# Optimization experiments

Hardware: AMD Instinct MI355X
Metric: run time of the kernel (lower is better)

## Reference

```python
import jax, jax.numpy as jnp
import numpy as np

B0, C0, H0, W0 = 32, 512, 64, 64  # x shape; L = C0 = d_model
DC = 32   # c_increase (per-direction inner dim)
NS = 16   # d_state
RK = 32   # dt_rank = ceil(512/16)


def setup_inputs() -> dict:
    key = jax.random.key(0)
    ks = jax.random.split(key, 8)
    x = jax.random.normal(ks[0], (B0, C0, H0, W0), jnp.float32)
    xc_proj_weight = jax.random.normal(ks[1], (2, RK + 2 * NS, DC), jnp.float32) * 0.05
    dtc_projs_weight = jax.random.uniform(ks[2], (2, DC, RK), jnp.float32, -RK ** -0.5, RK ** -0.5)
    # inv-softplus of dt sampled log-uniform in [1e-3, 1e-1]
    dt = jnp.exp(jax.random.uniform(ks[3], (2, DC)) * (np.log(0.1) - np.log(0.001)) + np.log(0.001))
    dtc_projs_bias = dt + jnp.log(-jnp.expm1(-dt))
    Ac_logs = jnp.log(jnp.tile(jnp.arange(1, NS + 1, dtype=jnp.float32), (2 * DC, 1)))  # [2D, N]
    Dcs = jnp.ones((2 * DC,), jnp.float32)
    w_cin = jax.random.normal(ks[4], (DC, 2), jnp.float32) * 0.5    # Conv2d(2, DC, 1) weight
    bn_gamma = jnp.ones((DC,), jnp.float32)
    bn_beta = jnp.zeros((DC,), jnp.float32)
    bn_mean = jnp.zeros((DC,), jnp.float32)
    bn_var = jnp.ones((DC,), jnp.float32)
    w_cout = jax.random.normal(ks[5], (DC,), jnp.float32) * 0.2     # Conv2d(DC, 1, 1) weight
    ln_gamma = jnp.ones((C0,), jnp.float32)
    ln_beta = jnp.zeros((C0,), jnp.float32)
    return dict(x=x, xc_proj_weight=xc_proj_weight, dtc_projs_weight=dtc_projs_weight,
                dtc_projs_bias=dtc_projs_bias, Ac_logs=Ac_logs, Dcs=Dcs, w_cin=w_cin,
                bn_gamma=bn_gamma, bn_beta=bn_beta, bn_mean=bn_mean, bn_var=bn_var,
                w_cout=w_cout, ln_gamma=ln_gamma, ln_beta=ln_beta)


def _selective_scan(u, delta, A, Bs, Cs, D, delta_bias):
    # u, delta: [B, 2D, L]; A: [2D, N]; Bs, Cs: [B, 2, N, L] (K=2 groups); D, delta_bias: [2D]
    B, KD, L = u.shape
    d_per = KD // Bs.shape[1]
    delta = jax.nn.softplus(delta + delta_bias[None, :, None])
    Bg = jnp.repeat(Bs, d_per, axis=1)  # [B, 2D, N, L] (group = d // d_per)
    Cg = jnp.repeat(Cs, d_per, axis=1)
    dA = jnp.exp(delta[:, :, None, :] * A[None, :, :, None])      # [B, 2D, N, L]
    dBu = delta[:, :, None, :] * Bg * u[:, :, None, :]            # [B, 2D, N, L]

    def step(h, inp):
        dA_l, dBu_l = inp
        h = dA_l * h + dBu_l
        return h, h

    h0 = jnp.zeros((B, KD, dA.shape[2]), u.dtype)
    _, hs = jax.lax.scan(step, h0, (jnp.moveaxis(dA, 3, 0), jnp.moveaxis(dBu, 3, 0)))  # [L, B, 2D, N]
    y = jnp.einsum('lbdn,bdnl->bdl', hs, Cg) + D[None, :, None] * u
    return y


def reference(x, xc_proj_weight, dtc_projs_weight, dtc_projs_bias, Ac_logs, Dcs,
              w_cin, bn_gamma, bn_beta, bn_mean, bn_var, w_cout, ln_gamma, ln_beta):
    B, C, H, W = x.shape
    L = C
    avg = jnp.mean(x, axis=(2, 3))          # [B, C]
    mx = jnp.max(x, axis=(2, 3))            # [B, C]
    xsc = jnp.stack([avg, mx], axis=1)       # [B, 2, C]
    # 1x1 conv (2 -> DC) over 'spatial' dim C, + BatchNorm(eval) + GELU
    h = jnp.einsum('bic,di->bdc', xsc, w_cin)  # [B, DC, L]
    h = (h - bn_mean[None, :, None]) * jax.lax.rsqrt(bn_var + 1e-5)[None, :, None]
    h = h * bn_gamma[None, :, None] + bn_beta[None, :, None]
    h = jax.nn.gelu(h, approximate=False)
    # bidirectional stacking
    xk = jnp.stack([h, jnp.flip(h, axis=-1)], axis=1)  # [B, 2, DC, L]
    dbl = jnp.einsum('bkdl,kcd->bkcl', xk, xc_proj_weight)  # [B, 2, R+2N, L]
    dts, Bs, Cs = dbl[:, :, :RK], dbl[:, :, RK:RK + NS], dbl[:, :, RK + NS:]
    dts = jnp.einsum('bkrl,kdr->bkdl', dts, dtc_projs_weight)  # [B, 2, DC, L]
    u = xk.reshape(B, 2 * DC, L)
    delta = dts.reshape(B, 2 * DC, L)
    A = -jnp.exp(Ac_logs)  # [2D, N]
    out_y = _selective_scan(u, delta, A, Bs, Cs, Dcs, dtc_projs_bias.reshape(-1))
    out_y = out_y.reshape(B, 2, DC, L)
    y = out_y[:, 0] + jnp.flip(out_y[:, 1], axis=-1)  # [B, DC, L]
    # 1x1 conv (DC -> 1, no bias) + GELU
    y = jax.nn.gelu(jnp.einsum('bdl,d->bl', y, w_cout), approximate=False)  # [B, L]
    # LayerNorm over channel dim (d_model = C)
    mu = jnp.mean(y, axis=-1, keepdims=True)
    var = jnp.var(y, axis=-1, keepdims=True)
    attn = (y - mu) * jax.lax.rsqrt(var + 1e-5) * ln_gamma[None, :] + ln_beta[None, :]
    attn = attn[:, :, None, None]  # [B, C, 1, 1]
    return x + x * attn
```

## Files before the change

kernel.cpp:

```cpp
#include <hip/hip_runtime.h>
#include <math.h>

#define B0 32
#define C0 512
#define HW 4096
#define DC 32
#define NS 16
#define RK 32
#define L  512
#define KD 64
#define CB 64
#define NCH (L / CB)
#define FSTR 16

#define LOAD_ACQ(p)    __hip_atomic_load((p), __ATOMIC_ACQUIRE, __HIP_MEMORY_SCOPE_AGENT)
#define LOAD_RLX(p)    __hip_atomic_load((p), __ATOMIC_RELAXED, __HIP_MEMORY_SCOPE_AGENT)
#define STORE_RLX(p,v) __hip_atomic_store((p), (v), __ATOMIC_RELAXED, __HIP_MEMORY_SCOPE_AGENT)
#define STORE_REL(p,v) __hip_atomic_store((p), (v), __ATOMIC_RELEASE, __HIP_MEMORY_SCOPE_AGENT)

__device__ __forceinline__ float gelu_exact(float x) {
    return 0.5f * x * (1.0f + erff(x * 0.70710678118654752f));
}
__device__ __forceinline__ float softplus_f(float x) {
    float ax = fabsf(x);
    return fmaxf(x, 0.0f) + log1pf(expf(-ax));
}

__global__ __launch_bounds__(256) void pool_kernel(const float* __restrict__ x,
                                                   float* __restrict__ avg,
                                                   float* __restrict__ mx) {
    int row = blockIdx.x;
    const float4* xr = (const float4*)(x + (size_t)row * HW);
    int tid = threadIdx.x;
    float s = 0.f, m = -INFINITY;
#pragma unroll
    for (int i = 0; i < 4; ++i) {
        float4 v = xr[tid + i * 256];
        s += v.x + v.y + v.z + v.w;
        m = fmaxf(m, fmaxf(fmaxf(v.x, v.y), fmaxf(v.z, v.w)));
    }
    for (int off = 32; off > 0; off >>= 1) {
        s += __shfl_down(s, off, 64);
        m = fmaxf(m, __shfl_down(m, off, 64));
    }
    __shared__ float ss[4], sm[4];
    int wave = tid >> 6;
    if ((tid & 63) == 0) { ss[wave] = s; sm[wave] = m; }
    __syncthreads();
    if (tid == 0) {
        s = ss[0] + ss[1] + ss[2] + ss[3];
        m = fmaxf(fmaxf(sm[0], sm[1]), fmaxf(sm[2], sm[3]));
        avg[row] = s * (1.0f / HW);
        mx[row] = m;
    }
}

__global__ __launch_bounds__(512) void mid_kernel(
    const float* __restrict__ avg, const float* __restrict__ mx,
    const float* __restrict__ w_cin,
    const float* __restrict__ bn_g, const float* __restrict__ bn_b,
    const float* __restrict__ bn_m, const float* __restrict__ bn_v,
    const float* __restrict__ xcw, const float* __restrict__ dtw,
    const float* __restrict__ dtb,
    const float* __restrict__ Ac_logs, const float* __restrict__ Dcs,
    const float* __restrict__ w_cout,
    float* __restrict__ carry,
    int* __restrict__ flags,
    float* __restrict__ ybl2)
{
    __shared__ float sW[64 * DC];
    __shared__ float sPW[DC * RK];
    __shared__ float sh_c[DC * (CB + 1)];
    __shared__ float sde[DC * (CB + 1)];
    __shared__ float sdtred[DC * (CB + 1)];
    __shared__ float sB[CB * (NS + 1)];
    __shared__ float sC[CB * (NS + 1)];

    float* sdt = sdtred;
    float* red = sdtred;

    int bk = blockIdx.x & 63;
    int c  = blockIdx.x >> 6;
    int k = bk & 1;
    int b = bk >> 1;
    int lidx = bk * NCH + c;
    int tid = threadIdx.x;

    for (int i = tid; i < 64 * DC; i += 512) sW[i]  = xcw[k * 64 * DC + i];
    for (int i = tid; i < DC * RK; i += 512) sPW[i] = dtw[k * DC * RK + i];

    int l0 = k ? (L - (c + 1) * CB) : c * CB;

    for (int i = tid; i < DC * CB; i += 512) {
        int d = i >> 6, ll = i & (CB - 1);
        int gl = l0 + ll;
        float a = avg[b * C0 + gl], m = mx[b * C0 + gl];
        float v = a * w_cin[d * 2] + m * w_cin[d * 2 + 1];
        v = (v - bn_m[d]) * rsqrtf(bn_v[d] + 1e-5f);
        v = v * bn_g[d] + bn_b[d];
        sh_c[d * (CB + 1) + ll] = gelu_exact(v);
    }
    __syncthreads();

    for (int idx = tid; idx < 64 * CB; idx += 512) {
        int cc = idx >> 6, ll = idx & (CB - 1);
        float acc = 0.f;
#pragma unroll
        for (int d = 0; d < DC; ++d) acc += sh_c[d * (CB + 1) + ll] * sW[cc * DC + d];
        if (cc < RK) sdt[cc * CB + ll] = acc;
        else if (cc < RK + NS) sB[ll * (NS + 1) + (cc - RK)] = acc;
        else sC[ll * (NS + 1) + (cc - RK - NS)] = acc;
    }
    __syncthreads();

    for (int idx = tid; idx < DC * CB; idx += 512) {
        int d = idx >> 6, ll = idx & (CB - 1);
        float acc = dtb[k * DC + d];
#pragma unroll
        for (int r = 0; r < RK; ++r) acc += sdt[r * CB + ll] * sPW[d * RK + r];
        sde[d * (CB + 1) + ll] = softplus_f(acc);
    }
    __syncthreads();

    int d_s = tid >> 4;
    int n_s = tid & 15;
    int kd  = k * DC + d_s;
    float A = -expf(Ac_logs[kd * NS + n_s]);
    float hloc = 0.f, sdsum = 0.f;
#pragma unroll 4
    for (int sl = 0; sl < CB; ++sl) {
        int ll = k ? (CB - 1 - sl) : sl;
        float de = sde[d_s * (CB + 1) + ll];
        float u  = sh_c[d_s * (CB + 1) + ll];
        float Bv = sB[ll * (NS + 1) + n_s];
        hloc = expf(de * A) * hloc + de * Bv * u;
        sdsum += de;
    }

    float cin = 0.f;
    if (c > 0) {
        const int* fprev = flags + (lidx - 1) * FSTR;
        if (tid == 0) {
            while (LOAD_ACQ(fprev) == 0) __builtin_amdgcn_s_sleep(2);
        }
        __syncthreads();
        cin = LOAD_RLX(carry + (size_t)(lidx - 1) * (DC * NS) + tid);
    }
    if (c < NCH - 1) {
        float cout = expf(A * sdsum) * cin + hloc;
        STORE_RLX(carry + (size_t)lidx * (DC * NS) + tid, cout);
        __syncthreads();
        if (tid == 0) STORE_REL(flags + lidx * FSTR, 1);
    }

    float w  = w_cout[d_s];
    float Dv = Dcs[kd];
    float hs = cin;
#pragma unroll 4
    for (int sl = 0; sl < CB; ++sl) {
        int ll = k ? (CB - 1 - sl) : sl;
        float de = sde[d_s * (CB + 1) + ll];
        float u  = sh_c[d_s * (CB + 1) + ll];
        float Bv = sB[ll * (NS + 1) + n_s];
        float Cv = sC[ll * (NS + 1) + n_s];
        hs = expf(de * A) * hs + de * Bv * u;
        float contrib = hs * Cv;
        contrib += __shfl_xor(contrib, 1, 16);
        contrib += __shfl_xor(contrib, 2, 16);
        contrib += __shfl_xor(contrib, 4, 16);
        contrib += __shfl_xor(contrib, 8, 16);
        if (n_s == 0) red[d_s * (CB + 1) + ll] = w * (contrib + Dv * u);
    }
    __syncthreads();

    if (tid < CB) {
        int ll = tid;
        float acc = 0.f;
#pragma unroll
        for (int dd = 0; dd < DC; ++dd) acc += red[dd * (CB + 1) + ll];
        ybl2[(size_t)bk * L + l0 + ll] = acc;
    }
}

__global__ __launch_bounds__(512) void epi_kernel(const float* __restrict__ ybl2,
                                                  const float* __restrict__ ln_g,
                                                  const float* __restrict__ ln_b,
                                                  float* __restrict__ attn) {
    int b = blockIdx.x;
    int l = threadIdx.x;
    float y = gelu_exact(ybl2[(size_t)(b * 2) * L + l] + ybl2[(size_t)(b * 2 + 1) * L + l]);
    float s = y, s2 = y * y;
    for (int off = 32; off > 0; off >>= 1) {
        s += __shfl_down(s, off, 64);
        s2 += __shfl_down(s2, off, 64);
    }
    __shared__ float ss[8], ss2[8];
    __shared__ float smu, srv;
    int wave = l >> 6;
    if ((l & 63) == 0) { ss[wave] = s; ss2[wave] = s2; }
    __syncthreads();
    if (l == 0) {
        float ts = 0.f, ts2 = 0.f;
#pragma unroll
        for (int i = 0; i < 8; ++i) { ts += ss[i]; ts2 += ss2[i]; }
        float mu = ts * (1.0f / L);
        float var = ts2 * (1.0f / L) - mu * mu;
        smu = mu;
        srv = rsqrtf(var + 1e-5f);
    }
    __syncthreads();
    attn[b * C0 + l] = (y - smu) * srv * ln_g[l] + ln_b[l];
}

__global__ __launch_bounds__(256) void gate_kernel(const float* __restrict__ x,
                                                   const float* __restrict__ attn,
                                                   float* __restrict__ out) {
    const float4* x4 = (const float4*)x;
    float4* o4 = (float4*)out;
    size_t base = (size_t)blockIdx.x * 2048 + threadIdx.x;
#pragma unroll
    for (int i = 0; i < 8; ++i) {
        size_t t = base + (size_t)i * 256;
        float4 v = x4[t];
        float a = 1.0f + attn[t >> 10];
        v.x *= a; v.y *= a; v.z *= a; v.w *= a;
        o4[t] = v;
    }
}

extern "C" void kernel_launch(void* const* d_in, const int* in_sizes, int n_in,
                              void* d_out, int out_size, void* d_ws, size_t ws_size,
                              hipStream_t stream) {
    const float* x     = (const float*)d_in[0];
    const float* xcw   = (const float*)d_in[1];
    const float* dtw   = (const float*)d_in[2];
    const float* dtb   = (const float*)d_in[3];
    const float* Aclog = (const float*)d_in[4];
    const float* Dcs   = (const float*)d_in[5];
    const float* wcin  = (const float*)d_in[6];
    const float* bng   = (const float*)d_in[7];
    const float* bnb   = (const float*)d_in[8];
    const float* bnm   = (const float*)d_in[9];
    const float* bnv   = (const float*)d_in[10];
    const float* wcout = (const float*)d_in[11];
    const float* lng   = (const float*)d_in[12];
    const float* lnb   = (const float*)d_in[13];
    float* out = (float*)d_out;

    float* ws = (float*)d_ws;
    float* avg   = ws;
    float* mx    = ws + 16384;
    float* ybl2  = ws + 32768;
    float* attn  = ws + 65536;
    float* carry = ws + 81920;
    int*   flags = (int*)(ws + 344064);

    pool_kernel<<<B0 * C0, 256, 0, stream>>>(x, avg, mx);
    hipMemsetAsync(flags, 0, (size_t)64 * NCH * FSTR * sizeof(int), stream);
    mid_kernel<<<64 * NCH, 512, 0, stream>>>(avg, mx, wcin, bng, bnb, bnm, bnv,
                                             xcw, dtw, dtb, Aclog, Dcs, wcout,
                                             carry, flags, ybl2);
    epi_kernel<<<B0, 512, 0, stream>>>(ybl2, lng, lnb, attn);
    gate_kernel<<<(B0 * C0 * HW / 4) / 2048, 256, 0, stream>>>(x, attn, out);
}
```

Measured before the change: 583.2 us.

## Replace serial chunk carry chain with independent publish and prefix recombination

Each chunk block now publishes its local end state and summed delta right away, without waiting for its predecessor. Consumers wait on all earlier chunk flags and rebuild the carry-in by combining those partial states in sequence. This removes the serial chunk-to-chunk dependency chain in the scan. The flag reset moves from a separate memset into the pool kernel, which drops one launch. In exchange, later chunks do more global loads and exps.

```diff
diff --git a/kernel.cpp b/kernel.cpp
--- a/kernel.cpp
+++ b/kernel.cpp
@@ -11,6 +11,7 @@
 #define KD 64
 #define CB 64
 #define NCH (L / CB)
+#define NBK 64
 #define FSTR 16
 
 #define LOAD_ACQ(p)    __hip_atomic_load((p), __ATOMIC_ACQUIRE, __HIP_MEMORY_SCOPE_AGENT)
@@ -28,8 +29,10 @@
 
 __global__ __launch_bounds__(256) void pool_kernel(const float* __restrict__ x,
                                                    float* __restrict__ avg,
-                                                   float* __restrict__ mx) {
+                                                   float* __restrict__ mx,
+                                                   int* __restrict__ flags) {
     int row = blockIdx.x;
+    if (row < NBK * NCH && threadIdx.x == 0) flags[row * FSTR] = 0;
     const float4* xr = (const float4*)(x + (size_t)row * HW);
     int tid = threadIdx.x;
     float s = 0.f, m = -INFINITY;
@@ -64,7 +67,8 @@
     const float* __restrict__ dtb,
     const float* __restrict__ Ac_logs, const float* __restrict__ Dcs,
     const float* __restrict__ w_cout,
-    float* __restrict__ carry,
+    float* __restrict__ hendg,
+    float* __restrict__ sdeg,
     int* __restrict__ flags,
     float* __restrict__ ybl2)
 {
@@ -79,11 +83,12 @@
     float* sdt = sdtred;
     float* red = sdtred;
 
-    int bk = blockIdx.x & 63;
+    int bk = blockIdx.x & (NBK - 1);
     int c  = blockIdx.x >> 6;
     int k = bk & 1;
     int b = bk >> 1;
-    int lidx = bk * NCH + c;
+    int base = bk * NCH;
+    int lidx = base + c;
     int tid = threadIdx.x;
 
     for (int i = tid; i < 64 * DC; i += 512) sW[i]  = xcw[k * 64 * DC + i];
@@ -137,20 +142,25 @@
         sdsum += de;
     }
 
+    if (c < NCH - 1) {
+        STORE_RLX(hendg + (size_t)lidx * (DC * NS) + tid, hloc);
+        if (n_s == 0) STORE_RLX(sdeg + lidx * DC + d_s, sdsum);
+        __syncthreads();
+        if (tid == 0) STORE_REL(flags + lidx * FSTR, 1);
+    }
+
     float cin = 0.f;
     if (c > 0) {
-        const int* fprev = flags + (lidx - 1) * FSTR;
-        if (tid == 0) {
-            while (LOAD_ACQ(fprev) == 0) __builtin_amdgcn_s_sleep(2);
+        if (tid < c) {
+            const int* fp = flags + (base + tid) * FSTR;
+            while (LOAD_ACQ(fp) == 0) __builtin_amdgcn_s_sleep(2);
         }
         __syncthreads();
-        cin = LOAD_RLX(carry + (size_t)(lidx - 1) * (DC * NS) + tid);
-    }
-    if (c < NCH - 1) {
-        float cout = expf(A * sdsum) * cin + hloc;
-        STORE_RLX(carry + (size_t)lidx * (DC * NS) + tid, cout);
-        __syncthreads();
-        if (tid == 0) STORE_REL(flags + lidx * FSTR, 1);
+        for (int j = 0; j < c; ++j) {
+            float sd = LOAD_RLX(sdeg + (base + j) * DC + d_s);
+            float he = LOAD_RLX(hendg + (size_t)(base + j) * (DC * NS) + tid);
+            cin = expf(A * sd) * cin + he;
+        }
     }
 
     float w  = w_cout[d_s];
@@ -252,14 +262,14 @@
     float* mx    = ws + 16384;
     float* ybl2  = ws + 32768;
     float* attn  = ws + 65536;
-    float* carry = ws + 81920;
-    int*   flags = (int*)(ws + 344064);
-
-    pool_kernel<<<B0 * C0, 256, 0, stream>>>(x, avg, mx);
-    hipMemsetAsync(flags, 0, (size_t)64 * NCH * FSTR * sizeof(int), stream);
-    mid_kernel<<<64 * NCH, 512, 0, stream>>>(avg, mx, wcin, bng, bnb, bnm, bnv,
-                                             xcw, dtw, dtb, Aclog, Dcs, wcout,
-                                             carry, flags, ybl2);
+    float* hendg = ws + 81920;
+    float* sdeg  = ws + 344064;
+    int*   flags = (int*)(ws + 360448);
+
+    pool_kernel<<<B0 * C0, 256, 0, stream>>>(x, avg, mx, flags);
+    mid_kernel<<<NBK * NCH, 512, 0, stream>>>(avg, mx, wcin, bng, bnb, bnm, bnv,
+                                              xcw, dtw, dtb, Aclog, Dcs, wcout,
+                                              hendg, sdeg, flags, ybl2);
     epi_kernel<<<B0, 512, 0, stream>>>(ybl2, lng, lnb, attn);
     gate_kernel<<<(B0 * C0 * HW / 4) / 2048, 256, 0, stream>>>(x, attn, out);
 }
```

New measurement: 553.1 us. -5.2%, faster.
